# Optimization experiments

Measured on AMD Instinct MI355X. Metric: run time of the kernel, lower is better.

Reference implementation:

```python
import jax, jax.numpy as jnp
import numpy as np

# ---- static config (Phi-3-small layer 0, blocksparse branch) ----
HIDDEN = 4096
N_HEADS = 32
N_KV = 8
HEAD_DIM = HIDDEN // N_HEADS        # 128
Q_PER_KV = N_HEADS // N_KV          # 4
SEQ = 2048
ROPE_BASE = 1000000.0
POS_SCALE = 1.0
SM_SCALE = 1.0 / HEAD_DIM           # mup scaling, multiplier=1.0
BLOCK = 64
LOCAL_BLOCKS = 16
VERT_STRIDE = 8


def _blocksparse_mask(seq_len):
    """Dense [S,S] bool mask realizing the causal blocksparse pattern:
    query block i attends key block j iff j<=i and (i-j < LOCAL_BLOCKS or (j+1) % VERT_STRIDE == 0),
    with elementwise causality inside blocks. Built once in numpy (static)."""
    nb = seq_len // BLOCK
    qb = np.arange(nb)[:, None]
    kb = np.arange(nb)[None, :]
    bmask = (kb <= qb) & ((qb - kb < LOCAL_BLOCKS) | ((kb + 1) % VERT_STRIDE == 0))
    emask = np.kron(bmask, np.ones((BLOCK, BLOCK), dtype=bool))
    i = np.arange(seq_len)
    emask &= i[:, None] >= i[None, :]
    return jnp.asarray(emask)


def _rope(x, cos, sin):
    # x: [B, S, H, D]; cos/sin: [S, D]
    x1, x2 = jnp.split(x, 2, axis=-1)
    rot = jnp.concatenate([-x2, x1], axis=-1)
    return x * cos[None, :, None, :] + rot * sin[None, :, None, :]


def setup_inputs() -> dict:
    key = jax.random.key(0)
    k1, k2, k3, k4, k5 = jax.random.split(key, 5)
    qkv_out = (N_HEADS + 2 * N_KV) * HEAD_DIM  # 6144
    return {
        "hidden_states": jax.random.normal(k1, (1, SEQ, HIDDEN), dtype=jnp.float32),
        "w_qkv": jax.random.normal(k2, (qkv_out, HIDDEN), dtype=jnp.float32) * 0.02,
        "b_qkv": jnp.zeros((qkv_out,), dtype=jnp.float32),
        "w_dense": jax.random.normal(k3, (HIDDEN, HIDDEN), dtype=jnp.float32) * 0.02,
        "b_dense": jnp.zeros((HIDDEN,), dtype=jnp.float32),
    }


def reference(hidden_states, w_qkv, b_qkv, w_dense, b_dense):
    B, S, _ = hidden_states.shape
    # grouped QKV projection: [B,S,(H+2*KV)*D]
    qkv = jnp.einsum("bsh,oh->bso", hidden_states, w_qkv) + b_qkv
    # group layout: (group, q0..q3, k, v) per kv head
    qkv = qkv.reshape(B, S, N_KV, Q_PER_KV + 2, HEAD_DIM)
    q = qkv[:, :, :, :Q_PER_KV].reshape(B, S, N_HEADS, HEAD_DIM)
    k = qkv[:, :, :, Q_PER_KV]   # [B,S,KV,D]
    v = qkv[:, :, :, Q_PER_KV + 1]
    # rotary embeddings (HF rotate-half style)
    inv_freq = 1.0 / (ROPE_BASE ** (jnp.arange(0, HEAD_DIM, 2, dtype=jnp.float32) / HEAD_DIM))
    t = jnp.arange(S, dtype=jnp.float32) * POS_SCALE
    freqs = jnp.outer(t, inv_freq)               # [S, D/2]
    emb = jnp.concatenate([freqs, freqs], axis=-1)
    cos, sin = jnp.cos(emb), jnp.sin(emb)
    q = _rope(q, cos, sin)
    k = _rope(k, cos, sin)
    # GQA: replicate kv heads to match q heads
    k = jnp.repeat(k, Q_PER_KV, axis=2)          # [B,S,H,D]
    v = jnp.repeat(v, Q_PER_KV, axis=2)
    mask = _blocksparse_mask(S)                  # [S,S] bool
    scores = jnp.einsum("bqhd,bkhd->bhqk", q, k) * SM_SCALE
    scores = jnp.where(mask[None, None], scores, jnp.finfo(scores.dtype).min)
    probs = jax.nn.softmax(scores, axis=-1)
    ctx = jnp.einsum("bhqk,bkhd->bqhd", probs, v).reshape(B, S, HIDDEN)
    out = jnp.einsum("bsh,oh->bso", ctx, w_dense) + b_dense
    return out
```

## Files before the change

kernel.cpp:

```cpp
#include <hip/hip_runtime.h>
#include <hip/hip_bf16.h>

#define SEQ 2048
#define HIDDEN 4096
#define NH 32
#define NKV 8
#define HD 128
#define QKV_OUT 6144
#define QSCALE (0.0078125f * 1.4426950408889634f)

typedef __attribute__((ext_vector_type(8))) short bf16x8;
typedef __attribute__((ext_vector_type(4))) float f32x4;
typedef __attribute__((ext_vector_type(16))) float f32x16;

__device__ inline unsigned short f32_bf16(float f) {
  union { float f; unsigned int u; } v; v.f = f;
  unsigned int r = v.u + 0x7FFFu + ((v.u >> 16) & 1u);
  return (unsigned short)(r >> 16);
}
__device__ inline unsigned int pk(float a, float b) {
  union { __hip_bfloat162 h; unsigned int u; } t;
  t.h = __float22bfloat162_rn(make_float2(a, b));
  return t.u;
}
__device__ inline void pswap(unsigned int &a, unsigned int &b) {
  auto r = __builtin_amdgcn_permlane32_swap((int)a, (int)b, false, false);
  a = (unsigned int)r[0]; b = (unsigned int)r[1];
}
__device__ inline float xmax32(float v) {
  int x = __builtin_bit_cast(int, v);
  auto r = __builtin_amdgcn_permlane32_swap(x, x, false, false);
  return fmaxf(__builtin_bit_cast(float, (int)r[0]), __builtin_bit_cast(float, (int)r[1]));
}
__device__ inline float xadd32(float v) {
  int x = __builtin_bit_cast(int, v);
  auto r = __builtin_amdgcn_permlane32_swap(x, x, false, false);
  return __builtin_bit_cast(float, (int)r[0]) + __builtin_bit_cast(float, (int)r[1]);
}

__global__ __launch_bounds__(256) void conv_bf16(const float* __restrict__ in,
                                                 unsigned short* __restrict__ out,
                                                 int n) {
  int i = (blockIdx.x * 256 + threadIdx.x) * 8;
  if (i + 8 > n) return;
  float4 a = *reinterpret_cast<const float4*>(in + i);
  float4 b = *reinterpret_cast<const float4*>(in + i + 4);
  unsigned short t[8];
  t[0] = f32_bf16(a.x); t[1] = f32_bf16(a.y); t[2] = f32_bf16(a.z); t[3] = f32_bf16(a.w);
  t[4] = f32_bf16(b.x); t[5] = f32_bf16(b.y); t[6] = f32_bf16(b.z); t[7] = f32_bf16(b.w);
  *reinterpret_cast<uint4*>(out + i) = *reinterpret_cast<uint4*>(t);
}

__global__ __launch_bounds__(256) void build_tab(float* __restrict__ ct,
                                                 float* __restrict__ st) {
  int idx = blockIdx.x * 256 + threadIdx.x;
  int s = idx >> 6, d = idx & 63;
  float inv = powf(1.0e6f, -(float)d * (1.0f / 64.0f));
  float f = (float)s * inv;
  ct[idx] = cosf(f);
  st[idx] = sinf(f);
}

template <int BM, int BN, int LA, int LB>
__global__ __launch_bounds__(512, 2) void gemm8(const unsigned short* __restrict__ A,
                                                const unsigned short* __restrict__ B,
                                                const float* __restrict__ bias,
                                                float* __restrict__ C,
                                                int M, int N, int K) {
  constexpr int MREP = BM / 32;
  constexpr int NREP = BN / 64;
  constexpr int HALF = (BM + BN) * 64;
  constexpr int BUF = HALF * 2;
  constexpr int LP = LA + LB;
  __shared__ __align__(16) char Lds[BUF * 2];

  const int tid = threadIdx.x;
  const int wave = tid >> 6, lane = tid & 63;
  const int wr = wave >> 2, wc = wave & 3;
  const int lrow = lane & 15, lgrp = lane >> 4;

  const int nwg = gridDim.x;
  const int wg0 = blockIdx.x;
  const int wg = (wg0 & 7) * (nwg >> 3) + (wg0 >> 3);
  const int ntx = N / BN;
  const int bm = (wg / ntx) * BM, bn = (wg % ntx) * BN;

  const int srow = lane >> 2;
  const int scol = ((lane & 3) ^ ((lane >= 32) ? 2 : 0)) * 8;
  const unsigned short* gA = A + (size_t)(bm + wave * (BM / 8) + srow) * K + scol;
  const unsigned short* gB = B + (size_t)(bn + wave * (BN / 8) + srow) * K + scol;
  const int ldsAw = wave * (BM / 8) * 64;
  const int ldsBw = BM * 64 + wave * (BN / 8) * 64;

  auto stage = [&](int bufb, int h, int k0) {
#pragma unroll
    for (int i = 0; i < LA; ++i)
      __builtin_amdgcn_global_load_lds(
          (const __attribute__((address_space(1))) unsigned int*)(gA + (size_t)(i * 16) * K + k0 + h * 32),
          (__attribute__((address_space(3))) unsigned int*)(Lds + bufb + h * HALF + ldsAw + i * 1024),
          16, 0, 0);
#pragma unroll
    for (int i = 0; i < LB; ++i)
      __builtin_amdgcn_global_load_lds(
          (const __attribute__((address_space(1))) unsigned int*)(gB + (size_t)(i * 16) * K + k0 + h * 32),
          (__attribute__((address_space(3))) unsigned int*)(Lds + bufb + h * HALF + ldsBw + i * 1024),
          16, 0, 0);
  };

  const int flip = ((lrow >> 3) & 1) << 5;
  const int aoff = (wr * (BM / 2) + lrow) * 64 + ((lgrp * 16) ^ flip);
  const int boff = BM * 64 + (wc * (BN / 4) + lrow) * 64 + ((lgrp * 16) ^ flip);

  f32x4 acc[MREP][NREP] = {};

  auto phase = [&](int cur, int h) {
    const char* base = Lds + cur + h * HALF;
    bf16x8 af[MREP], bfr[NREP];
#pragma unroll
    for (int m = 0; m < MREP; ++m)
      af[m] = *reinterpret_cast<const bf16x8*>(base + aoff + m * 1024);
#pragma unroll
    for (int n = 0; n < NREP; ++n)
      bfr[n] = *reinterpret_cast<const bf16x8*>(base + boff + n * 1024);
    __builtin_amdgcn_s_setprio(1);
#pragma unroll
    for (int m = 0; m < MREP; ++m)
#pragma unroll
      for (int n = 0; n < NREP; ++n)
        acc[m][n] = __builtin_amdgcn_mfma_f32_16x16x32_bf16(af[m], bfr[n], acc[m][n], 0, 0, 0);
    __builtin_amdgcn_s_setprio(0);
  };

  const int nt = K / 64;
  stage(0, 0, 0);
  stage(0, 1, 0);
  for (int t = 0; t < nt - 1; ++t) {
    const int cur = (t & 1) ? BUF : 0;
    const int nxt = cur ^ BUF;
    const int k1 = (t + 1) * 64;
#pragma unroll
    for (int h = 0; h < 2; ++h) {
      stage(nxt, h, k1);
      if constexpr (LP == 4) asm volatile("s_waitcnt vmcnt(8)" ::: "memory");
      else                   asm volatile("s_waitcnt vmcnt(6)" ::: "memory");
      __builtin_amdgcn_s_barrier();
      asm volatile("" ::: "memory");
      phase(cur, h);
    }
  }
  {
    const int cur = ((nt - 1) & 1) ? BUF : 0;
    if constexpr (LP == 4) asm volatile("s_waitcnt vmcnt(4)" ::: "memory");
    else                   asm volatile("s_waitcnt vmcnt(3)" ::: "memory");
    __builtin_amdgcn_s_barrier();
    asm volatile("" ::: "memory");
    phase(cur, 0);
    asm volatile("s_waitcnt vmcnt(0)" ::: "memory");
    __builtin_amdgcn_s_barrier();
    asm volatile("" ::: "memory");
    phase(cur, 1);
  }

#pragma unroll
  for (int n = 0; n < NREP; ++n) {
    int col = bn + wc * (BN / 4) + n * 16 + lrow;
    float bv = bias[col];
#pragma unroll
    for (int m = 0; m < MREP; ++m)
#pragma unroll
      for (int r = 0; r < 4; ++r) {
        int row = bm + wr * (BM / 2) + m * 16 + lgrp * 4 + r;
        C[(size_t)row * N + col] = acc[m][n][r] + bv;
      }
  }
}

__global__ __launch_bounds__(256) void rope_split(const float* __restrict__ qkv,
                                                  const float* __restrict__ ct,
                                                  const float* __restrict__ st,
                                                  unsigned short* __restrict__ Q,
                                                  unsigned short* __restrict__ Kh,
                                                  unsigned short* __restrict__ Vt) {
  int idx = blockIdx.x * 256 + threadIdx.x;
  int d = idx & 127;
  int t = idx >> 7;
  int head = t % 48;
  int s = t / 48;
  int gg = head / 6, slot = head - gg * 6;
  const float* base = qkv + (size_t)s * QKV_OUT + gg * 768 + slot * 128;
  float x = base[d];
  if (slot == 5) {
    Vt[((size_t)gg * HD + d) * SEQ + s] = f32_bf16(x);
  } else {
    int dm = d & 63;
    float c = ct[s * 64 + dm], sn = st[s * 64 + dm];
    float rot = (d < 64) ? -base[d + 64] : base[d - 64];
    float val = x * c + rot * sn;
    if (slot < 4)
      Q[((size_t)(gg * 4 + slot) * SEQ + s) * HD + d] = f32_bf16(val * QSCALE);
    else
      Kh[((size_t)gg * SEQ + s) * HD + d] = f32_bf16(val);
  }
}

__device__ inline int nextj(int x, int qb) {
  if (x > qb) return -1;
  if (qb - x < 16) return x;
  int v = (x & ~7) + 7;
  int w = qb - 15;
  return v < w ? v : w;
}

__global__ __launch_bounds__(256, 2) void attn32(const unsigned short* __restrict__ Q,
                                                 const unsigned short* __restrict__ Kh,
                                                 const unsigned short* __restrict__ Vt,
                                                 unsigned short* __restrict__ ctx) {
  const int g = blockIdx.x;
  const int y = (int)gridDim.y - 1 - (int)blockIdx.y;
  const int qb = y >> 1, half = y & 1;
  const int Q0 = y * 32;
  const int tid = threadIdx.x;
  const int wave = tid >> 6;
  const int h = g * 4 + wave;
  const int lane = tid & 63;
  const int l31 = lane & 31, hi = lane >> 5;

  __shared__ __align__(16) char Lds[65536];

  auto stage = [&](int bufb, int j) {
#pragma unroll
    for (int i = 0; i < 4; ++i) {
      int row = i * 16 + (tid >> 4);
      const unsigned short* src =
          Kh + ((size_t)(g * SEQ + j * 64 + row)) * HD + ((tid & 15) ^ (row & 15)) * 8;
      __builtin_amdgcn_global_load_lds(
          (const __attribute__((address_space(1))) unsigned int*)src,
          (__attribute__((address_space(3))) unsigned int*)(Lds + bufb + i * 4096 + (tid >> 6) * 1024),
          16, 0, 0);
    }
#pragma unroll
    for (int i = 0; i < 4; ++i) {
      int row = i * 32 + (tid >> 3);
      const unsigned short* src =
          Vt + ((size_t)(g * HD + row)) * SEQ + j * 64 + ((tid & 7) ^ (row & 7)) * 8;
      __builtin_amdgcn_global_load_lds(
          (const __attribute__((address_space(1))) unsigned int*)src,
          (__attribute__((address_space(3))) unsigned int*)(Lds + bufb + 16384 + i * 4096 + (tid >> 6) * 1024),
          16, 0, 0);
    }
  };

  bf16x8 qf[8];
  const unsigned short* qbase = Q + ((size_t)h * SEQ + Q0 + l31) * HD;
#pragma unroll
  for (int kk = 0; kk < 8; ++kk)
    qf[kk] = *reinterpret_cast<const bf16x8*>(qbase + kk * 16 + hi * 8);

  f32x16 ot[4] = {};
  float mrow = -1e30f, lsum = 0.f;

  const int kswz = l31 & 15;
  const int vswz = l31 & 7;

  int j = nextj(0, qb);
  int cur = 0;
  stage(0, j);
  asm volatile("s_waitcnt vmcnt(0)" ::: "memory");
  __builtin_amdgcn_sched_barrier(0);
  __builtin_amdgcn_s_barrier();
  __builtin_amdgcn_sched_barrier(0);

  while (true) {
    const int jn = (j < qb) ? nextj(j + 1, qb) : -1;
    if (jn >= 0) stage(cur ^ 32768, jn);

    const char* kb = Lds + cur;
    const char* vb = Lds + cur + 16384;
    const bool diag = (j == qb);
    const bool short_blk = diag && (half == 0);

    f32x16 st[2] = {};
    __builtin_amdgcn_s_setprio(1);
#pragma unroll
    for (int kk = 0; kk < 8; ++kk) {
      bf16x8 k0 = *reinterpret_cast<const bf16x8*>(
          kb + (size_t)l31 * 256 + (((2 * kk + hi) ^ kswz) * 16));
      st[0] = __builtin_amdgcn_mfma_f32_32x32x16_bf16(k0, qf[kk], st[0], 0, 0, 0);
      if (!short_blk) {
        bf16x8 k1 = *reinterpret_cast<const bf16x8*>(
            kb + (size_t)(32 + l31) * 256 + (((2 * kk + hi) ^ kswz) * 16));
        st[1] = __builtin_amdgcn_mfma_f32_32x32x16_bf16(k1, qf[kk], st[1], 0, 0, 0);
      }
    }
    __builtin_amdgcn_s_setprio(0);

    if (diag) {
      int qrel = half * 32 + l31;
#pragma unroll
      for (int kt = 0; kt < 2; ++kt)
#pragma unroll
        for (int r = 0; r < 16; ++r) {
          int krel = kt * 32 + (r & 3) + 8 * (r >> 2) + 4 * hi;
          if (krel > qrel) st[kt][r] = -1e30f;
        }
    }

    float t16[16];
#pragma unroll
    for (int r = 0; r < 16; ++r) t16[r] = fmaxf(st[0][r], st[1][r]);
#pragma unroll
    for (int sft = 8; sft >= 1; sft >>= 1)
#pragma unroll
      for (int r = 0; r < sft; ++r) t16[r] = fmaxf(t16[r], t16[r + sft]);
    float vm = xmax32(t16[0]);

    if (!__all(vm - mrow <= 8.0f)) {
      float nm = fmaxf(mrow, vm);
      float corr = __builtin_amdgcn_exp2f(mrow - nm);
      lsum *= corr;
#pragma unroll
      for (int dt = 0; dt < 4; ++dt)
#pragma unroll
        for (int r = 0; r < 16; ++r) ot[dt][r] *= corr;
      mrow = nm;
    }

    float s4[4] = {0.f, 0.f, 0.f, 0.f};
#pragma unroll
    for (int kt = 0; kt < 2; ++kt)
#pragma unroll
      for (int r = 0; r < 16; ++r) {
        float p = __builtin_amdgcn_exp2f(st[kt][r] - mrow);
        st[kt][r] = p;
        s4[r & 3] += p;
      }
    lsum += xadd32((s4[0] + s4[1]) + (s4[2] + s4[3]));

    bf16x8 pb[4];
#pragma unroll
    for (int s = 0; s < 4; ++s) {
      int kt = s >> 1, g0 = (s & 1) * 2, g1 = g0 + 1;
      unsigned int a0 = pk(st[kt][4 * g0 + 0], st[kt][4 * g0 + 1]);
      unsigned int a1 = pk(st[kt][4 * g0 + 2], st[kt][4 * g0 + 3]);
      unsigned int b0 = pk(st[kt][4 * g1 + 0], st[kt][4 * g1 + 1]);
      unsigned int b1 = pk(st[kt][4 * g1 + 2], st[kt][4 * g1 + 3]);
      pswap(a0, b0);
      pswap(a1, b1);
      union { unsigned int u[4]; bf16x8 v; } t;
      t.u[0] = a0; t.u[1] = a1; t.u[2] = b0; t.u[3] = b1;
      pb[s] = t.v;
    }

    const int smax = short_blk ? 2 : 4;
    __builtin_amdgcn_s_setprio(1);
#pragma unroll
    for (int dt = 0; dt < 4; ++dt) {
      const char* vrow = vb + (size_t)(dt * 32 + l31) * 128;
#pragma unroll
      for (int s = 0; s < 4; ++s)
        if (s < smax)
          ot[dt] = __builtin_amdgcn_mfma_f32_32x32x16_bf16(
              *reinterpret_cast<const bf16x8*>(vrow + (((2 * s + hi) ^ vswz) * 16)),
              pb[s], ot[dt], 0, 0, 0);
    }
    __builtin_amdgcn_s_setprio(0);

    if (jn < 0) break;
    asm volatile("s_waitcnt vmcnt(0)" ::: "memory");
    __builtin_amdgcn_sched_barrier(0);
    __builtin_amdgcn_s_barrier();
    __builtin_amdgcn_sched_barrier(0);
    j = jn;
    cur ^= 32768;
  }

  __syncthreads();
  char* W = Lds + wave * 8192;
  float inv = 1.0f / lsum;
  const int swz = (l31 & 7) << 4;
#pragma unroll
  for (int dt = 0; dt < 4; ++dt)
#pragma unroll
    for (int gg = 0; gg < 4; ++gg) {
      unsigned int u0 = pk(ot[dt][4 * gg + 0] * inv, ot[dt][4 * gg + 1] * inv);
      unsigned int u1 = pk(ot[dt][4 * gg + 2] * inv, ot[dt][4 * gg + 3] * inv);
      int off = (dt * 64 + gg * 16 + hi * 8) ^ swz;
      *reinterpret_cast<uint2*>(W + l31 * 256 + off) = make_uint2(u0, u1);
    }
#pragma unroll
  for (int i = 0; i < 8; ++i) {
    int row = lane >> 1;
    int t = (lane & 1) * 8 + i;
    bf16x8 vv = *reinterpret_cast<const bf16x8*>(
        W + row * 256 + ((t * 16) ^ ((row & 7) << 4)));
    *reinterpret_cast<bf16x8*>(&ctx[(size_t)(Q0 + row) * HIDDEN + h * HD + t * 8]) = vv;
  }
}

extern "C" void kernel_launch(void* const* d_in, const int* in_sizes, int n_in,
                              void* d_out, int out_size, void* d_ws, size_t ws_size,
                              hipStream_t stream) {
  const float* hidden  = (const float*)d_in[0];
  const float* w_qkv   = (const float*)d_in[1];
  const float* b_qkv   = (const float*)d_in[2];
  const float* w_dense = (const float*)d_in[3];
  const float* b_dense = (const float*)d_in[4];
  float* out = (float*)d_out;

  char* p = (char*)d_ws;
  unsigned short* hid_bf  = (unsigned short*)p; p += (size_t)SEQ * HIDDEN * 2;
  unsigned short* wqkv_bf = (unsigned short*)p; p += (size_t)QKV_OUT * HIDDEN * 2;
  unsigned short* wd_bf   = (unsigned short*)p; p += (size_t)HIDDEN * HIDDEN * 2;
  float* qkv              = (float*)p;          p += (size_t)SEQ * QKV_OUT * 4;
  unsigned short* Qb      = (unsigned short*)p; p += (size_t)NH * SEQ * HD * 2;
  unsigned short* Kb      = (unsigned short*)p; p += (size_t)NKV * SEQ * HD * 2;
  unsigned short* Vt      = (unsigned short*)p; p += (size_t)NKV * HD * SEQ * 2;
  float* ct               = (float*)p;          p += (size_t)SEQ * 64 * 4;
  float* st               = (float*)p;          p += (size_t)SEQ * 64 * 4;
  unsigned short* ctx = hid_bf;

  conv_bf16<<<(SEQ * HIDDEN) / 2048, 256, 0, stream>>>(hidden, hid_bf, SEQ * HIDDEN);
  conv_bf16<<<(QKV_OUT * HIDDEN) / 2048, 256, 0, stream>>>(w_qkv, wqkv_bf, QKV_OUT * HIDDEN);
  conv_bf16<<<(HIDDEN * HIDDEN) / 2048, 256, 0, stream>>>(w_dense, wd_bf, HIDDEN * HIDDEN);
  build_tab<<<(SEQ * 64) / 256, 256, 0, stream>>>(ct, st);

  gemm8<256, 256, 2, 2><<<dim3((SEQ / 256) * (QKV_OUT / 256)), 512, 0, stream>>>(
      hid_bf, wqkv_bf, b_qkv, qkv, SEQ, QKV_OUT, HIDDEN);
  rope_split<<<(SEQ * 48 * 128) / 256, 256, 0, stream>>>(qkv, ct, st, Qb, Kb, Vt);
  attn32<<<dim3(NKV, SEQ / 32), 256, 0, stream>>>(Qb, Kb, Vt, ctx);
  gemm8<128, 256, 1, 2><<<dim3((SEQ / 128) * (HIDDEN / 256)), 512, 0, stream>>>(
      ctx, wd_bf, b_dense, out, SEQ, HIDDEN, HIDDEN);
}
```

Before: 302.5 us.

## Store QKV in bf16, vectorize rope/V-transpose, XCD-aware tile mapping, split MFMA phase

The QKV GEMM now writes a bf16 intermediate instead of fp32, which halves the traffic between the GEMM and the rope kernel. The rope kernel is rewritten to handle 8 elements per thread with vector loads and stores. The V transpose moves to a separate block range that gathers 8 sequence positions per thread so the store is 16 bytes wide. Both GEMMs remap workgroups so that each XCD gets a compact rectangle of tiles for better L2 reuse, and the MFMA phase is split in half with an extra barrier and explicit lgkmcnt waits. Rounding QKV to bf16 before rope adds a small accuracy loss, and the extra barrier per phase may cost sync time.

```diff
diff --git a/kernel.cpp b/kernel.cpp
--- a/kernel.cpp
+++ b/kernel.cpp
@@ -17,6 +17,10 @@
   union { float f; unsigned int u; } v; v.f = f;
   unsigned int r = v.u + 0x7FFFu + ((v.u >> 16) & 1u);
   return (unsigned short)(r >> 16);
+}
+__device__ inline float bf16_f32(unsigned short u) {
+  union { unsigned int u; float f; } v; v.u = (unsigned int)u << 16;
+  return v.f;
 }
 __device__ inline unsigned int pk(float a, float b) {
   union { __hip_bfloat162 h; unsigned int u; } t;
@@ -61,14 +65,15 @@
   st[idx] = sinf(f);
 }
 
-template <int BM, int BN, int LA, int LB>
+template <int BM, int BN, int LA, int LB, int CR, int CC, bool OBF>
 __global__ __launch_bounds__(512, 2) void gemm8(const unsigned short* __restrict__ A,
                                                 const unsigned short* __restrict__ B,
                                                 const float* __restrict__ bias,
-                                                float* __restrict__ C,
+                                                void* __restrict__ Cp,
                                                 int M, int N, int K) {
   constexpr int MREP = BM / 32;
   constexpr int NREP = BN / 64;
+  constexpr int MH = MREP / 2;
   constexpr int HALF = (BM + BN) * 64;
   constexpr int BUF = HALF * 2;
   constexpr int LP = LA + LB;
@@ -79,11 +84,15 @@
   const int wr = wave >> 2, wc = wave & 3;
   const int lrow = lane & 15, lgrp = lane >> 4;
 
-  const int nwg = gridDim.x;
+  const int ntx = N / BN;
   const int wg0 = blockIdx.x;
-  const int wg = (wg0 & 7) * (nwg >> 3) + (wg0 >> 3);
-  const int ntx = N / BN;
-  const int bm = (wg / ntx) * BM, bn = (wg % ntx) * BN;
+  const int xcd = wg0 & 7, w = wg0 >> 3;
+  constexpr int CPB = 0;
+  const int cpb = ntx / CC;
+  const int band = xcd / cpb, colc = xcd % cpb;
+  const int bmi = band * CR + w / CC;
+  const int bni = colc * CC + w % CC;
+  const int bm = bmi * BM, bn = bni * BN;
 
   const int srow = lane >> 2;
   const int scol = ((lane & 3) ^ ((lane >= 32) ? 2 : 0)) * 8;
@@ -117,14 +126,30 @@
     const char* base = Lds + cur + h * HALF;
     bf16x8 af[MREP], bfr[NREP];
 #pragma unroll
-    for (int m = 0; m < MREP; ++m)
+    for (int m = 0; m < MH; ++m)
       af[m] = *reinterpret_cast<const bf16x8*>(base + aoff + m * 1024);
 #pragma unroll
     for (int n = 0; n < NREP; ++n)
       bfr[n] = *reinterpret_cast<const bf16x8*>(base + boff + n * 1024);
+    asm volatile("s_waitcnt lgkmcnt(0)" ::: "memory");
+    __builtin_amdgcn_sched_barrier(0);
     __builtin_amdgcn_s_setprio(1);
 #pragma unroll
-    for (int m = 0; m < MREP; ++m)
+    for (int m = 0; m < MH; ++m)
+#pragma unroll
+      for (int n = 0; n < NREP; ++n)
+        acc[m][n] = __builtin_amdgcn_mfma_f32_16x16x32_bf16(af[m], bfr[n], acc[m][n], 0, 0, 0);
+    __builtin_amdgcn_s_setprio(0);
+    __builtin_amdgcn_sched_barrier(0);
+#pragma unroll
+    for (int m = MH; m < MREP; ++m)
+      af[m] = *reinterpret_cast<const bf16x8*>(base + aoff + m * 1024);
+    __builtin_amdgcn_s_barrier();
+    asm volatile("s_waitcnt lgkmcnt(0)" ::: "memory");
+    __builtin_amdgcn_sched_barrier(0);
+    __builtin_amdgcn_s_setprio(1);
+#pragma unroll
+    for (int m = MH; m < MREP; ++m)
 #pragma unroll
       for (int n = 0; n < NREP; ++n)
         acc[m][n] = __builtin_amdgcn_mfma_f32_16x16x32_bf16(af[m], bfr[n], acc[m][n], 0, 0, 0);
@@ -170,36 +195,62 @@
 #pragma unroll
       for (int r = 0; r < 4; ++r) {
         int row = bm + wr * (BM / 2) + m * 16 + lgrp * 4 + r;
-        C[(size_t)row * N + col] = acc[m][n][r] + bv;
+        if constexpr (OBF)
+          ((unsigned short*)Cp)[(size_t)row * N + col] = f32_bf16(acc[m][n][r] + bv);
+        else
+          ((float*)Cp)[(size_t)row * N + col] = acc[m][n][r] + bv;
       }
   }
 }
 
-__global__ __launch_bounds__(256) void rope_split(const float* __restrict__ qkv,
+__global__ __launch_bounds__(256) void rope_split(const unsigned short* __restrict__ qkvb,
                                                   const float* __restrict__ ct,
                                                   const float* __restrict__ st,
                                                   unsigned short* __restrict__ Q,
                                                   unsigned short* __restrict__ Kh,
                                                   unsigned short* __restrict__ Vt) {
-  int idx = blockIdx.x * 256 + threadIdx.x;
-  int d = idx & 127;
-  int t = idx >> 7;
-  int head = t % 48;
-  int s = t / 48;
-  int gg = head / 6, slot = head - gg * 6;
-  const float* base = qkv + (size_t)s * QKV_OUT + gg * 768 + slot * 128;
-  float x = base[d];
-  if (slot == 5) {
-    Vt[((size_t)gg * HD + d) * SEQ + s] = f32_bf16(x);
+  int b = blockIdx.x;
+  if (b < 5120) {
+    int t = b * 256 + threadIdx.x;
+    int d8 = (t & 15) * 8;
+    int q = t >> 4;
+    int s = q / 40;
+    int slotg = q - s * 40;
+    int g = slotg / 5, slot = slotg - g * 5;
+    const unsigned short* base = qkvb + (size_t)s * QKV_OUT + g * 768 + slot * 128;
+    bf16x8 x8 = *reinterpret_cast<const bf16x8*>(base + d8);
+    bf16x8 r8 = *reinterpret_cast<const bf16x8*>(base + (d8 ^ 64));
+    float4 c0 = *reinterpret_cast<const float4*>(ct + s * 64 + (d8 & 63));
+    float4 c1 = *reinterpret_cast<const float4*>(ct + s * 64 + (d8 & 63) + 4);
+    float4 s0 = *reinterpret_cast<const float4*>(st + s * 64 + (d8 & 63));
+    float4 s1 = *reinterpret_cast<const float4*>(st + s * 64 + (d8 & 63) + 4);
+    float cc[8] = {c0.x, c0.y, c0.z, c0.w, c1.x, c1.y, c1.z, c1.w};
+    float ss[8] = {s0.x, s0.y, s0.z, s0.w, s1.x, s1.y, s1.z, s1.w};
+    float sgn = (d8 < 64) ? -1.0f : 1.0f;
+    float sc = (slot < 4) ? QSCALE : 1.0f;
+    unsigned short o[8];
+#pragma unroll
+    for (int i = 0; i < 8; ++i) {
+      float x = bf16_f32((unsigned short)x8[i]);
+      float r = bf16_f32((unsigned short)r8[i]) * sgn;
+      o[i] = f32_bf16((x * cc[i] + r * ss[i]) * sc);
+    }
+    unsigned short* dst = (slot < 4)
+        ? Q + ((size_t)(g * 4 + slot) * SEQ + s) * HD + d8
+        : Kh + ((size_t)g * SEQ + s) * HD + d8;
+    *reinterpret_cast<uint4*>(dst) = *reinterpret_cast<uint4*>(o);
   } else {
-    int dm = d & 63;
-    float c = ct[s * 64 + dm], sn = st[s * 64 + dm];
-    float rot = (d < 64) ? -base[d + 64] : base[d - 64];
-    float val = x * c + rot * sn;
-    if (slot < 4)
-      Q[((size_t)(gg * 4 + slot) * SEQ + s) * HD + d] = f32_bf16(val * QSCALE);
-    else
-      Kh[((size_t)gg * SEQ + s) * HD + d] = f32_bf16(val);
+    int t2 = (b - 5120) * 256 + threadIdx.x;
+    int d = t2 & 127;
+    int rest = t2 >> 7;
+    int g = rest & 7;
+    int s0 = (rest >> 3) * 8;
+    const unsigned short* src = qkvb + (size_t)s0 * QKV_OUT + g * 768 + 640 + d;
+    unsigned short o[8];
+#pragma unroll
+    for (int i = 0; i < 8; ++i) o[i] = src[(size_t)i * QKV_OUT];
+    *reinterpret_cast<uint4*>(&Vt[((size_t)g * HD + d) * SEQ + s0]) =
+        *reinterpret_cast<uint4*>(o);
   }
 }
 
@@ -411,7 +462,7 @@
   unsigned short* hid_bf  = (unsigned short*)p; p += (size_t)SEQ * HIDDEN * 2;
   unsigned short* wqkv_bf = (unsigned short*)p; p += (size_t)QKV_OUT * HIDDEN * 2;
   unsigned short* wd_bf   = (unsigned short*)p; p += (size_t)HIDDEN * HIDDEN * 2;
-  float* qkv              = (float*)p;          p += (size_t)SEQ * QKV_OUT * 4;
+  unsigned short* qkvb    = (unsigned short*)p; p += (size_t)SEQ * QKV_OUT * 2;
   unsigned short* Qb      = (unsigned short*)p; p += (size_t)NH * SEQ * HD * 2;
   unsigned short* Kb      = (unsigned short*)p; p += (size_t)NKV * SEQ * HD * 2;
   unsigned short* Vt      = (unsigned short*)p; p += (size_t)NKV * HD * SEQ * 2;
@@ -424,10 +475,12 @@
   conv_bf16<<<(HIDDEN * HIDDEN) / 2048, 256, 0, stream>>>(w_dense, wd_bf, HIDDEN * HIDDEN);
   build_tab<<<(SEQ * 64) / 256, 256, 0, stream>>>(ct, st);
 
-  gemm8<256, 256, 2, 2><<<dim3((SEQ / 256) * (QKV_OUT / 256)), 512, 0, stream>>>(
-      hid_bf, wqkv_bf, b_qkv, qkv, SEQ, QKV_OUT, HIDDEN);
-  rope_split<<<(SEQ * 48 * 128) / 256, 256, 0, stream>>>(qkv, ct, st, Qb, Kb, Vt);
+  gemm8<256, 256, 2, 2, 4, 6, true>
+      <<<dim3((SEQ / 256) * (QKV_OUT / 256)), 512, 0, stream>>>(
+          hid_bf, wqkv_bf, b_qkv, qkvb, SEQ, QKV_OUT, HIDDEN);
+  rope_split<<<5120 + 1024, 256, 0, stream>>>(qkvb, ct, st, Qb, Kb, Vt);
   attn32<<<dim3(NKV, SEQ / 32), 256, 0, stream>>>(Qb, Kb, Vt, ctx);
-  gemm8<128, 256, 1, 2><<<dim3((SEQ / 128) * (HIDDEN / 256)), 512, 0, stream>>>(
-      ctx, wd_bf, b_dense, out, SEQ, HIDDEN, HIDDEN);
-}
+  gemm8<128, 256, 1, 2, 8, 4, false>
+      <<<dim3((SEQ / 128) * (HIDDEN / 256)), 512, 0, stream>>>(
+          ctx, wd_bf, b_dense, out, SEQ, HIDDEN, HIDDEN);
+}
```

Result: faster. 287.8 us (median of 2 runs) (-4.9%).
